# Optimization experiments

Hardware: AMD Instinct MI355X
Metric: run time of the kernel (lower is better)

The kernel has to match this reference:

```python
import jax, jax.numpy as jnp
import numpy as np

B, S, D = 16384, 50, 256
H2 = D // 2  # att_fc1 output = hidden_size // 2

def setup_inputs() -> dict:
    key = jax.random.key(0)
    k1, k2, k3, k4, k5, k6 = jax.random.split(key, 6)
    user_news_vecs = jax.random.normal(k1, (B, S, D), dtype=jnp.float32)
    log_mask = jax.random.randint(k2, (B, S), 0, 2, dtype=jnp.int32)
    # learned params
    pad_doc = jax.random.uniform(k3, (1, D), dtype=jnp.float32, minval=-1.0, maxval=1.0)
    lim1 = 1.0 / np.sqrt(D)
    W1 = jax.random.uniform(k4, (D, H2), dtype=jnp.float32, minval=-lim1, maxval=lim1)
    b1 = jnp.zeros((H2,), dtype=jnp.float32)
    lim2 = 1.0 / np.sqrt(H2)
    W2 = jax.random.uniform(k5, (H2, 1), dtype=jnp.float32, minval=-lim2, maxval=lim2)
    b2 = jnp.zeros((1,), dtype=jnp.float32)
    return {"user_news_vecs": user_news_vecs, "log_mask": log_mask,
            "pad_doc": pad_doc, "W1": W1, "b1": b1, "W2": W2, "b2": b2}

def reference(user_news_vecs, log_mask, pad_doc, W1, b1, W2, b2):
    # use_mask=False branch of get_user_log_vec: replace masked-out slots with pad_doc
    m = log_mask.astype(user_news_vecs.dtype)[..., None]          # [B,S,1]
    x = user_news_vecs * m + pad_doc[None, :, :] * (1.0 - m)      # [B,S,D]
    # AttentionPooling with attn_mask=None
    e = jnp.tanh(jnp.einsum('bsd,dh->bsh', x, W1) + b1)           # [B,S,H2]
    alpha = jnp.exp(jnp.einsum('bsh,ho->bso', e, W2) + b2)        # [B,S,1]
    alpha = alpha / (jnp.sum(alpha, axis=1, keepdims=True) + 1e-8)
    out = jnp.einsum('bsd,bso->bd', x, alpha)                     # [B,D]
    return out
```

## Files before the change

### kernel.cpp

```cpp
#include <hip/hip_runtime.h>

#define BB 16384
#define SS 50
#define DD 256
#define HH 128

typedef __attribute__((ext_vector_type(8))) __bf16 bf16x8;
typedef __attribute__((ext_vector_type(4))) float f32x4;

__global__ __launch_bounds__(256) void prep_w1(const float* __restrict__ W1,
                                               __bf16* __restrict__ w1t) {
    int idx = blockIdx.x * 256 + threadIdx.x;
    int n = idx >> 8;
    int k = idx & 255;
    w1t[n * 256 + k] = (__bf16)W1[k * HH + n];
}

template <bool USE_WS>
__global__ __launch_bounds__(256, 4) void user_enc(
    const float* __restrict__ vecs,
    const int*   __restrict__ lmask,
    const float* __restrict__ pad,
    const float* __restrict__ b1,
    const float* __restrict__ W2,
    const float* __restrict__ b2,
    const __bf16* __restrict__ w1t,
    const float* __restrict__ W1f,
    float* __restrict__ out)
{
    __shared__ float s_alpha[SS];
    __shared__ float s_m[SS];
    __shared__ __align__(16) float s_part[256 * 4];
    __shared__ float s_sum[4], s_pad[4];

    const int b    = blockIdx.x;
    const int t    = threadIdx.x;
    const int wid  = t >> 6;
    const int lane = t & 63;
    const int lo16 = lane & 15;
    const int q    = lane >> 4;
    const int r    = (wid << 4) + lo16;

    bool act = false;
    if (r < SS) act = (lmask[b * SS + r] != 0);
    if (q == 0 && r < SS) s_m[r] = act ? 1.0f : 0.0f;

    const float* vrowp = vecs + (size_t)b * (SS * DD) + (size_t)r * DD;
    bf16x8 afr[8];
    #pragma unroll
    for (int kk = 0; kk < 8; ++kk) {
        const float* src = pad + kk * 32 + q * 8;
        float4 lo = *(const float4*)(src);
        float4 hi = *(const float4*)(src + 4);
        bf16x8 f;
        f[0] = (__bf16)lo.x; f[1] = (__bf16)lo.y; f[2] = (__bf16)lo.z; f[3] = (__bf16)lo.w;
        f[4] = (__bf16)hi.x; f[5] = (__bf16)hi.y; f[6] = (__bf16)hi.z; f[7] = (__bf16)hi.w;
        afr[kk] = f;
    }
    if (act) {
        #pragma unroll
        for (int kk = 0; kk < 8; ++kk) {
            const float* src = vrowp + kk * 32 + q * 8;
            float4 lo = *(const float4*)(src);
            float4 hi = *(const float4*)(src + 4);
            bf16x8 f;
            f[0] = (__bf16)lo.x; f[1] = (__bf16)lo.y; f[2] = (__bf16)lo.z; f[3] = (__bf16)lo.w;
            f[4] = (__bf16)hi.x; f[5] = (__bf16)hi.y; f[6] = (__bf16)hi.z; f[7] = (__bf16)hi.w;
            afr[kk] = f;
        }
    }

    const float b2v = b2[0];
    float zacc[4] = {0.f, 0.f, 0.f, 0.f};

    #pragma unroll
    for (int nt = 0; nt < 8; ++nt) {
        const int c = (nt << 4) + lo16;
        f32x4 acc = {0.f, 0.f, 0.f, 0.f};
        #pragma unroll
        for (int kk = 0; kk < 8; ++kk) {
            bf16x8 bfr;
            if constexpr (USE_WS) {
                bfr = *(const bf16x8*)(w1t + c * 256 + kk * 32 + q * 8);
            } else {
                #pragma unroll
                for (int j = 0; j < 8; ++j)
                    bfr[j] = (__bf16)W1f[(kk * 32 + q * 8 + j) * HH + c];
            }
            acc = __builtin_amdgcn_mfma_f32_16x16x32_bf16(afr[kk], bfr, acc, 0, 0, 0);
        }
        const float b1c = b1[c];
        const float w2c = W2[c];
        #pragma unroll
        for (int i = 0; i < 4; ++i) {
            float y = acc[i] + b1c;
            y = fminf(fmaxf(y, -15.f), 15.f);
            float ex = __expf(2.f * y);
            float th = (ex - 1.f) * __builtin_amdgcn_rcpf(ex + 1.f);
            zacc[i] += th * w2c;
        }
    }

    #pragma unroll
    for (int i = 0; i < 4; ++i) {
        float z = zacc[i];
        z += __shfl_xor(z, 1);
        z += __shfl_xor(z, 2);
        z += __shfl_xor(z, 4);
        z += __shfl_xor(z, 8);
        if (lo16 == 0) {
            int srow = (wid << 4) + (q << 2) + i;
            if (srow < SS) s_alpha[srow] = __expf(z + b2v);
        }
    }
    __syncthreads();

    float4 acc4 = {0.f, 0.f, 0.f, 0.f};
    float asum = 0.f, apad = 0.f;
    const float* vb = vecs + (size_t)b * (SS * DD);
    for (int s = wid; s < SS; s += 4) {
        float a = s_alpha[s];
        asum += a;
        if (s_m[s] != 0.0f) {
            float4 xv = *(const float4*)(vb + s * DD + lane * 4);
            acc4.x += a * xv.x;
            acc4.y += a * xv.y;
            acc4.z += a * xv.z;
            acc4.w += a * xv.w;
        } else {
            apad += a;
        }
    }
    *(float4*)&s_part[t * 4] = acc4;
    if (lane == 0) { s_sum[wid] = asum; s_pad[wid] = apad; }
    __syncthreads();

    if (t < 64) {
        float4 p0 = *(const float4*)&s_part[(0 * 64 + t) * 4];
        float4 p1 = *(const float4*)&s_part[(1 * 64 + t) * 4];
        float4 p2 = *(const float4*)&s_part[(2 * 64 + t) * 4];
        float4 p3 = *(const float4*)&s_part[(3 * 64 + t) * 4];
        float denom = s_sum[0] + s_sum[1] + s_sum[2] + s_sum[3] + 1e-8f;
        float ptot  = s_pad[0] + s_pad[1] + s_pad[2] + s_pad[3];
        float inv = 1.0f / denom;
        float4 pd = *(const float4*)(pad + t * 4);
        float4 o;
        o.x = (p0.x + p1.x + p2.x + p3.x + ptot * pd.x) * inv;
        o.y = (p0.y + p1.y + p2.y + p3.y + ptot * pd.y) * inv;
        o.z = (p0.z + p1.z + p2.z + p3.z + ptot * pd.z) * inv;
        o.w = (p0.w + p1.w + p2.w + p3.w + ptot * pd.w) * inv;
        *(float4*)(out + (size_t)b * DD + t * 4) = o;
    }
}

extern "C" void kernel_launch(void* const* d_in, const int* in_sizes, int n_in,
                              void* d_out, int out_size, void* d_ws, size_t ws_size,
                              hipStream_t stream) {
    const float* vecs  = (const float*)d_in[0];
    const int*   lmask = (const int*)d_in[1];
    const float* pad   = (const float*)d_in[2];
    const float* W1    = (const float*)d_in[3];
    const float* b1    = (const float*)d_in[4];
    const float* W2    = (const float*)d_in[5];
    const float* b2    = (const float*)d_in[6];
    float* out = (float*)d_out;

    if (ws_size >= (size_t)(HH * DD * sizeof(__bf16))) {
        __bf16* w1t = (__bf16*)d_ws;
        prep_w1<<<dim3(HH * DD / 256), dim3(256), 0, stream>>>(W1, w1t);
        user_enc<true><<<dim3(BB), dim3(256), 0, stream>>>(vecs, lmask, pad, b1, W2, b2,
                                                           w1t, W1, out);
    } else {
        user_enc<false><<<dim3(BB), dim3(256), 0, stream>>>(vecs, lmask, pad, b1, W2, b2,
                                                            nullptr, W1, out);
    }
}
```

Baseline: 1.416 ms.

## Process batches in pairs per block with persistent loop, precomputed pad alpha, prefetch

Each block now walks 16 batch rows in pairs instead of handling one row, so every W1 fragment load feeds two MFMAs. The attention logit for pad rows is computed once by a small prep kernel and substituted directly, which skips loading pad vectors into the A fragments. The next pair's vecs rows are touched early to warm the cache. The costs are higher register pressure from the doubled accumulators and fragments, and a grid 16x smaller, which may reduce latency hiding.

```diff
diff --git a/kernel.cpp b/kernel.cpp
--- a/kernel.cpp
+++ b/kernel.cpp
@@ -4,6 +4,8 @@
 #define SS 50
 #define DD 256
 #define HH 128
+#define NB 16
+#define GRID (BB / NB)
 
 typedef __attribute__((ext_vector_type(8))) __bf16 bf16x8;
 typedef __attribute__((ext_vector_type(4))) float f32x4;
@@ -14,6 +16,24 @@
     int n = idx >> 8;
     int k = idx & 255;
     w1t[n * 256 + k] = (__bf16)W1[k * HH + n];
+}
+
+__global__ __launch_bounds__(128) void prep_pad(const float* __restrict__ pad,
+                                                const float* __restrict__ W1,
+                                                const float* __restrict__ b1,
+                                                const float* __restrict__ W2,
+                                                const float* __restrict__ b2,
+                                                float* __restrict__ apad) {
+    __shared__ float s2[2];
+    const int h = threadIdx.x;
+    float a = b1[h];
+    for (int k = 0; k < DD; ++k) a = fmaf(pad[k], W1[k * HH + h], a);
+    float v = tanhf(a) * W2[h];
+    #pragma unroll
+    for (int off = 1; off < 64; off <<= 1) v += __shfl_xor(v, off);
+    if ((h & 63) == 0) s2[h >> 6] = v;
+    __syncthreads();
+    if (h == 0) apad[0] = __expf(s2[0] + s2[1] + b2[0]);
 }
 
 template <bool USE_WS>
@@ -26,14 +46,14 @@
     const float* __restrict__ b2,
     const __bf16* __restrict__ w1t,
     const float* __restrict__ W1f,
+    const float* __restrict__ apad_ws,
     float* __restrict__ out)
 {
-    __shared__ float s_alpha[SS];
-    __shared__ float s_m[SS];
-    __shared__ __align__(16) float s_part[256 * 4];
-    __shared__ float s_sum[4], s_pad[4];
-
-    const int b    = blockIdx.x;
+    __shared__ float s_alpha[2][SS];
+    __shared__ float s_m[2][SS];
+    __shared__ __align__(16) float s_part[2][256 * 4];
+    __shared__ float s_sum[2][4], s_pad2[2][4];
+
     const int t    = threadIdx.x;
     const int wid  = t >> 6;
     const int lane = t & 63;
@@ -41,115 +61,196 @@
     const int q    = lane >> 4;
     const int r    = (wid << 4) + lo16;
 
-    bool act = false;
-    if (r < SS) act = (lmask[b * SS + r] != 0);
-    if (q == 0 && r < SS) s_m[r] = act ? 1.0f : 0.0f;
-
-    const float* vrowp = vecs + (size_t)b * (SS * DD) + (size_t)r * DD;
-    bf16x8 afr[8];
+    const float b2v   = b2[0];
+    const float apadv = USE_WS ? apad_ws[0] : 0.0f;
+    const int   bbase = blockIdx.x * NB;
+
+    bool act[2];
     #pragma unroll
-    for (int kk = 0; kk < 8; ++kk) {
-        const float* src = pad + kk * 32 + q * 8;
-        float4 lo = *(const float4*)(src);
-        float4 hi = *(const float4*)(src + 4);
-        bf16x8 f;
-        f[0] = (__bf16)lo.x; f[1] = (__bf16)lo.y; f[2] = (__bf16)lo.z; f[3] = (__bf16)lo.w;
-        f[4] = (__bf16)hi.x; f[5] = (__bf16)hi.y; f[6] = (__bf16)hi.z; f[7] = (__bf16)hi.w;
-        afr[kk] = f;
-    }
-    if (act) {
-        #pragma unroll
-        for (int kk = 0; kk < 8; ++kk) {
-            const float* src = vrowp + kk * 32 + q * 8;
-            float4 lo = *(const float4*)(src);
-            float4 hi = *(const float4*)(src + 4);
-            bf16x8 f;
-            f[0] = (__bf16)lo.x; f[1] = (__bf16)lo.y; f[2] = (__bf16)lo.z; f[3] = (__bf16)lo.w;
-            f[4] = (__bf16)hi.x; f[5] = (__bf16)hi.y; f[6] = (__bf16)hi.z; f[7] = (__bf16)hi.w;
-            afr[kk] = f;
-        }
-    }
-
-    const float b2v = b2[0];
-    float zacc[4] = {0.f, 0.f, 0.f, 0.f};
-
-    #pragma unroll
-    for (int nt = 0; nt < 8; ++nt) {
-        const int c = (nt << 4) + lo16;
-        f32x4 acc = {0.f, 0.f, 0.f, 0.f};
-        #pragma unroll
-        for (int kk = 0; kk < 8; ++kk) {
-            bf16x8 bfr;
+    for (int u = 0; u < 2; ++u)
+        act[u] = (r < SS) && (lmask[(size_t)(bbase + u) * SS + r] != 0);
+
+    for (int p = 0; p < NB / 2; ++p) {
+        const int b = bbase + 2 * p;
+        const float* vb0 = vecs + (size_t)b * (SS * DD);
+        const float* vb1 = vb0 + SS * DD;
+
+        bf16x8 afr[2][8];
+        #pragma unroll
+        for (int u = 0; u < 2; ++u) {
+            const float* vrowp = (u ? vb1 : vb0) + (size_t)r * DD;
             if constexpr (USE_WS) {
-                bfr = *(const bf16x8*)(w1t + c * 256 + kk * 32 + q * 8);
+                #pragma unroll
+                for (int kk = 0; kk < 8; ++kk) {
+                    bf16x8 f;
+                    #pragma unroll
+                    for (int j = 0; j < 8; ++j) f[j] = (__bf16)0.0f;
+                    afr[u][kk] = f;
+                }
+                if (act[u]) {
+                    #pragma unroll
+                    for (int kk = 0; kk < 8; ++kk) {
+                        const float* src = vrowp + kk * 32 + q * 8;
+                        float4 lo = *(const float4*)(src);
+                        float4 hi = *(const float4*)(src + 4);
+                        bf16x8 f;
+                        f[0] = (__bf16)lo.x; f[1] = (__bf16)lo.y; f[2] = (__bf16)lo.z; f[3] = (__bf16)lo.w;
+                        f[4] = (__bf16)hi.x; f[5] = (__bf16)hi.y; f[6] = (__bf16)hi.z; f[7] = (__bf16)hi.w;
+                        afr[u][kk] = f;
+                    }
+                }
             } else {
                 #pragma unroll
-                for (int j = 0; j < 8; ++j)
-                    bfr[j] = (__bf16)W1f[(kk * 32 + q * 8 + j) * HH + c];
-            }
-            acc = __builtin_amdgcn_mfma_f32_16x16x32_bf16(afr[kk], bfr, acc, 0, 0, 0);
-        }
-        const float b1c = b1[c];
-        const float w2c = W2[c];
+                for (int kk = 0; kk < 8; ++kk) {
+                    const float* src = pad + kk * 32 + q * 8;
+                    float4 lo = *(const float4*)(src);
+                    float4 hi = *(const float4*)(src + 4);
+                    bf16x8 f;
+                    f[0] = (__bf16)lo.x; f[1] = (__bf16)lo.y; f[2] = (__bf16)lo.z; f[3] = (__bf16)lo.w;
+                    f[4] = (__bf16)hi.x; f[5] = (__bf16)hi.y; f[6] = (__bf16)hi.z; f[7] = (__bf16)hi.w;
+                    afr[u][kk] = f;
+                }
+                if (act[u]) {
+                    #pragma unroll
+                    for (int kk = 0; kk < 8; ++kk) {
+                        const float* src = vrowp + kk * 32 + q * 8;
+                        float4 lo = *(const float4*)(src);
+                        float4 hi = *(const float4*)(src + 4);
+                        bf16x8 f;
+                        f[0] = (__bf16)lo.x; f[1] = (__bf16)lo.y; f[2] = (__bf16)lo.z; f[3] = (__bf16)lo.w;
+                        f[4] = (__bf16)hi.x; f[5] = (__bf16)hi.y; f[6] = (__bf16)hi.z; f[7] = (__bf16)hi.w;
+                        afr[u][kk] = f;
+                    }
+                }
+            }
+        }
+        if (q == 0 && r < SS) {
+            s_m[0][r] = act[0] ? 1.0f : 0.0f;
+            s_m[1][r] = act[1] ? 1.0f : 0.0f;
+        }
+
+        bool actn[2] = {false, false};
+        float tch[8] = {0.f, 0.f, 0.f, 0.f, 0.f, 0.f, 0.f, 0.f};
+        if (p + 1 < NB / 2) {
+            #pragma unroll
+            for (int u = 0; u < 2; ++u) {
+                actn[u] = (r < SS) && (lmask[(size_t)(b + 2 + u) * SS + r] != 0);
+                if (actn[u]) {
+                    const float* vn = vecs + (size_t)(b + 2 + u) * (SS * DD) + (size_t)r * DD;
+                    #pragma unroll
+                    for (int j = 0; j < 4; ++j)
+                        tch[u * 4 + j] = vn[(q * 4 + j) * 16];
+                }
+            }
+        }
+
+        float zacc[2][4] = {{0.f,0.f,0.f,0.f},{0.f,0.f,0.f,0.f}};
+        #pragma unroll
+        for (int nt = 0; nt < 8; ++nt) {
+            const int c = (nt << 4) + lo16;
+            f32x4 acc0 = {0.f,0.f,0.f,0.f};
+            f32x4 acc1 = {0.f,0.f,0.f,0.f};
+            #pragma unroll
+            for (int kk = 0; kk < 8; ++kk) {
+                bf16x8 bfr;
+                if constexpr (USE_WS) {
+                    bfr = *(const bf16x8*)(w1t + c * 256 + kk * 32 + q * 8);
+                } else {
+                    #pragma unroll
+                    for (int j = 0; j < 8; ++j)
+                        bfr[j] = (__bf16)W1f[(kk * 32 + q * 8 + j) * HH + c];
+                }
+                acc0 = __builtin_amdgcn_mfma_f32_16x16x32_bf16(afr[0][kk], bfr, acc0, 0, 0, 0);
+                acc1 = __builtin_amdgcn_mfma_f32_16x16x32_bf16(afr[1][kk], bfr, acc1, 0, 0, 0);
+            }
+            const float b1c = b1[c];
+            const float w2c = W2[c];
+            #pragma unroll
+            for (int i = 0; i < 4; ++i) {
+                {
+                    float y = acc0[i] + b1c;
+                    y = fminf(fmaxf(y, -15.f), 15.f);
+                    float ex = __expf(2.f * y);
+                    zacc[0][i] += (ex - 1.f) * __builtin_amdgcn_rcpf(ex + 1.f) * w2c;
+                }
+                {
+                    float y = acc1[i] + b1c;
+                    y = fminf(fmaxf(y, -15.f), 15.f);
+                    float ex = __expf(2.f * y);
+                    zacc[1][i] += (ex - 1.f) * __builtin_amdgcn_rcpf(ex + 1.f) * w2c;
+                }
+            }
+        }
+
+        const float actf0 = act[0] ? 1.f : 0.f;
+        const float actf1 = act[1] ? 1.f : 0.f;
         #pragma unroll
         for (int i = 0; i < 4; ++i) {
-            float y = acc[i] + b1c;
-            y = fminf(fmaxf(y, -15.f), 15.f);
-            float ex = __expf(2.f * y);
-            float th = (ex - 1.f) * __builtin_amdgcn_rcpf(ex + 1.f);
-            zacc[i] += th * w2c;
-        }
-    }
-
-    #pragma unroll
-    for (int i = 0; i < 4; ++i) {
-        float z = zacc[i];
-        z += __shfl_xor(z, 1);
-        z += __shfl_xor(z, 2);
-        z += __shfl_xor(z, 4);
-        z += __shfl_xor(z, 8);
-        if (lo16 == 0) {
-            int srow = (wid << 4) + (q << 2) + i;
-            if (srow < SS) s_alpha[srow] = __expf(z + b2v);
-        }
-    }
-    __syncthreads();
-
-    float4 acc4 = {0.f, 0.f, 0.f, 0.f};
-    float asum = 0.f, apad = 0.f;
-    const float* vb = vecs + (size_t)b * (SS * DD);
-    for (int s = wid; s < SS; s += 4) {
-        float a = s_alpha[s];
-        asum += a;
-        if (s_m[s] != 0.0f) {
-            float4 xv = *(const float4*)(vb + s * DD + lane * 4);
-            acc4.x += a * xv.x;
-            acc4.y += a * xv.y;
-            acc4.z += a * xv.z;
-            acc4.w += a * xv.w;
-        } else {
-            apad += a;
-        }
-    }
-    *(float4*)&s_part[t * 4] = acc4;
-    if (lane == 0) { s_sum[wid] = asum; s_pad[wid] = apad; }
-    __syncthreads();
-
-    if (t < 64) {
-        float4 p0 = *(const float4*)&s_part[(0 * 64 + t) * 4];
-        float4 p1 = *(const float4*)&s_part[(1 * 64 + t) * 4];
-        float4 p2 = *(const float4*)&s_part[(2 * 64 + t) * 4];
-        float4 p3 = *(const float4*)&s_part[(3 * 64 + t) * 4];
-        float denom = s_sum[0] + s_sum[1] + s_sum[2] + s_sum[3] + 1e-8f;
-        float ptot  = s_pad[0] + s_pad[1] + s_pad[2] + s_pad[3];
-        float inv = 1.0f / denom;
-        float4 pd = *(const float4*)(pad + t * 4);
-        float4 o;
-        o.x = (p0.x + p1.x + p2.x + p3.x + ptot * pd.x) * inv;
-        o.y = (p0.y + p1.y + p2.y + p3.y + ptot * pd.y) * inv;
-        o.z = (p0.z + p1.z + p2.z + p3.z + ptot * pd.z) * inv;
-        o.w = (p0.w + p1.w + p2.w + p3.w + ptot * pd.w) * inv;
-        *(float4*)(out + (size_t)b * DD + t * 4) = o;
+            float z0 = zacc[0][i], z1 = zacc[1][i];
+            z0 += __shfl_xor(z0, 1); z0 += __shfl_xor(z0, 2);
+            z0 += __shfl_xor(z0, 4); z0 += __shfl_xor(z0, 8);
+            z1 += __shfl_xor(z1, 1); z1 += __shfl_xor(z1, 2);
+            z1 += __shfl_xor(z1, 4); z1 += __shfl_xor(z1, 8);
+            const int srow = (wid << 4) + (q << 2) + i;
+            const float a0 = __shfl(actf0, (q << 2) + i);
+            const float a1 = __shfl(actf1, (q << 2) + i);
+            if (lo16 == 0 && srow < SS) {
+                if constexpr (USE_WS) {
+                    s_alpha[0][srow] = (a0 != 0.f) ? __expf(z0 + b2v) : apadv;
+                    s_alpha[1][srow] = (a1 != 0.f) ? __expf(z1 + b2v) : apadv;
+                } else {
+                    s_alpha[0][srow] = __expf(z0 + b2v);
+                    s_alpha[1][srow] = __expf(z1 + b2v);
+                }
+            }
+        }
+
+        asm volatile("" :: "v"(tch[0]), "v"(tch[1]), "v"(tch[2]), "v"(tch[3]),
+                           "v"(tch[4]), "v"(tch[5]), "v"(tch[6]), "v"(tch[7]));
+        __syncthreads();
+
+        #pragma unroll
+        for (int u = 0; u < 2; ++u) {
+            const float* vbu = u ? vb1 : vb0;
+            float4 acc4 = {0.f, 0.f, 0.f, 0.f};
+            float asum = 0.f, apacc = 0.f;
+            for (int s = wid; s < SS; s += 4) {
+                float a = s_alpha[u][s];
+                asum += a;
+                if (s_m[u][s] != 0.0f) {
+                    float4 xv = *(const float4*)(vbu + s * DD + lane * 4);
+                    acc4.x += a * xv.x;
+                    acc4.y += a * xv.y;
+                    acc4.z += a * xv.z;
+                    acc4.w += a * xv.w;
+                } else {
+                    apacc += a;
+                }
+            }
+            *(float4*)&s_part[u][t * 4] = acc4;
+            if (lane == 0) { s_sum[u][wid] = asum; s_pad2[u][wid] = apacc; }
+        }
+        __syncthreads();
+
+        if (wid < 2) {
+            const int u = wid;
+            float4 p0 = *(const float4*)&s_part[u][(0 * 64 + lane) * 4];
+            float4 p1 = *(const float4*)&s_part[u][(1 * 64 + lane) * 4];
+            float4 p2 = *(const float4*)&s_part[u][(2 * 64 + lane) * 4];
+            float4 p3 = *(const float4*)&s_part[u][(3 * 64 + lane) * 4];
+            float denom = s_sum[u][0] + s_sum[u][1] + s_sum[u][2] + s_sum[u][3] + 1e-8f;
+            float ptot  = s_pad2[u][0] + s_pad2[u][1] + s_pad2[u][2] + s_pad2[u][3];
+            float inv = 1.0f / denom;
+            float4 pd = *(const float4*)(pad + lane * 4);
+            float4 o;
+            o.x = (p0.x + p1.x + p2.x + p3.x + ptot * pd.x) * inv;
+            o.y = (p0.y + p1.y + p2.y + p3.y + ptot * pd.y) * inv;
+            o.z = (p0.z + p1.z + p2.z + p3.z + ptot * pd.z) * inv;
+            o.w = (p0.w + p1.w + p2.w + p3.w + ptot * pd.w) * inv;
+            *(float4*)(out + (size_t)(b + u) * DD + lane * 4) = o;
+        }
+        act[0] = actn[0];
+        act[1] = actn[1];
     }
 }
 
@@ -165,13 +266,16 @@
     const float* b2    = (const float*)d_in[6];
     float* out = (float*)d_out;
 
-    if (ws_size >= (size_t)(HH * DD * sizeof(__bf16))) {
+    const size_t w1t_bytes = (size_t)HH * DD * sizeof(__bf16);
+    if (ws_size >= w1t_bytes + 16) {
         __bf16* w1t = (__bf16*)d_ws;
+        float*  apad = (float*)((char*)d_ws + w1t_bytes);
         prep_w1<<<dim3(HH * DD / 256), dim3(256), 0, stream>>>(W1, w1t);
-        user_enc<true><<<dim3(BB), dim3(256), 0, stream>>>(vecs, lmask, pad, b1, W2, b2,
-                                                           w1t, W1, out);
+        prep_pad<<<dim3(1), dim3(128), 0, stream>>>(pad, W1, b1, W2, b2, apad);
+        user_enc<true><<<dim3(GRID), dim3(256), 0, stream>>>(vecs, lmask, pad, b1, W2, b2,
+                                                             w1t, W1, apad, out);
     } else {
-        user_enc<false><<<dim3(BB), dim3(256), 0, stream>>>(vecs, lmask, pad, b1, W2, b2,
-                                                            nullptr, W1, out);
+        user_enc<false><<<dim3(GRID), dim3(256), 0, stream>>>(vecs, lmask, pad, b1, W2, b2,
+                                                              nullptr, W1, nullptr, out);
     }
 }
```

Result: slower. 1.853 ms (+30.9%).

## Process 16 batches per block with register-resident W1 and LDS-staged X tiles

Applied to the files above, without the earlier changes.

Each block now loops over 16 batch rows. W1 fragments stay in registers for the whole block, and each batch row's X is staged as bf16 in swizzled LDS. Each wave computes 32 hidden columns across all 64 padded rows, which removes the repeated per-block W1 loads. Masked rows skip the global read and use a precomputed pad-row alpha produced by a new tiny kernel. The cost is a large LDS footprint (about 32KB bf16 tile), lower occupancy, and more synchronisation inside each batch iteration.

```diff
diff --git a/kernel.cpp b/kernel.cpp
--- a/kernel.cpp
+++ b/kernel.cpp
@@ -4,6 +4,8 @@
 #define SS 50
 #define DD 256
 #define HH 128
+#define NB 16
+#define GRID (BB / NB)
 
 typedef __attribute__((ext_vector_type(8))) __bf16 bf16x8;
 typedef __attribute__((ext_vector_type(4))) float f32x4;
@@ -16,8 +18,26 @@
     w1t[n * 256 + k] = (__bf16)W1[k * HH + n];
 }
 
+__global__ __launch_bounds__(128) void prep_pad(const float* __restrict__ pad,
+                                                const float* __restrict__ W1,
+                                                const float* __restrict__ b1,
+                                                const float* __restrict__ W2,
+                                                const float* __restrict__ b2,
+                                                float* __restrict__ apad) {
+    __shared__ float s2[2];
+    const int h = threadIdx.x;
+    float a = b1[h];
+    for (int k = 0; k < DD; ++k) a = fmaf(pad[k], W1[k * HH + h], a);
+    float v = tanhf(a) * W2[h];
+    #pragma unroll
+    for (int off = 1; off < 64; off <<= 1) v += __shfl_xor(v, off);
+    if ((h & 63) == 0) s2[h >> 6] = v;
+    __syncthreads();
+    if (h == 0) apad[0] = __expf(s2[0] + s2[1] + b2[0]);
+}
+
 template <bool USE_WS>
-__global__ __launch_bounds__(256, 4) void user_enc(
+__global__ __launch_bounds__(256) void user_enc(
     const float* __restrict__ vecs,
     const int*   __restrict__ lmask,
     const float* __restrict__ pad,
@@ -26,130 +46,167 @@
     const float* __restrict__ b2,
     const __bf16* __restrict__ w1t,
     const float* __restrict__ W1f,
+    const float* __restrict__ apad_ws,
     float* __restrict__ out)
 {
-    __shared__ float s_alpha[SS];
-    __shared__ float s_m[SS];
+    __shared__ __align__(16) __bf16 s_x[64 * 256];
+    __shared__ float s_z[4][64];
+    __shared__ float s_alpha[64];
+    __shared__ float s_m[64];
     __shared__ __align__(16) float s_part[256 * 4];
-    __shared__ float s_sum[4], s_pad[4];
-
-    const int b    = blockIdx.x;
+    __shared__ float s_sum[4], s_apad[4];
+
     const int t    = threadIdx.x;
     const int wid  = t >> 6;
     const int lane = t & 63;
     const int lo16 = lane & 15;
     const int q    = lane >> 4;
-    const int r    = (wid << 4) + lo16;
-
-    bool act = false;
-    if (r < SS) act = (lmask[b * SS + r] != 0);
-    if (q == 0 && r < SS) s_m[r] = act ? 1.0f : 0.0f;
-
-    const float* vrowp = vecs + (size_t)b * (SS * DD) + (size_t)r * DD;
-    bf16x8 afr[8];
-    #pragma unroll
-    for (int kk = 0; kk < 8; ++kk) {
-        const float* src = pad + kk * 32 + q * 8;
-        float4 lo = *(const float4*)(src);
-        float4 hi = *(const float4*)(src + 4);
-        bf16x8 f;
-        f[0] = (__bf16)lo.x; f[1] = (__bf16)lo.y; f[2] = (__bf16)lo.z; f[3] = (__bf16)lo.w;
-        f[4] = (__bf16)hi.x; f[5] = (__bf16)hi.y; f[6] = (__bf16)hi.z; f[7] = (__bf16)hi.w;
-        afr[kk] = f;
-    }
-    if (act) {
+
+    const float b2v   = b2[0];
+    const float apadv = USE_WS ? apad_ws[0] : 0.0f;
+
+    const int c0 = wid * 32 + lo16;
+    const int c1 = c0 + 16;
+    const float b1c0 = b1[c0], b1c1 = b1[c1];
+    const float w2c0 = W2[c0], w2c1 = W2[c1];
+
+    bf16x8 bfr0[8], bfr1[8];
+    if constexpr (USE_WS) {
         #pragma unroll
         for (int kk = 0; kk < 8; ++kk) {
-            const float* src = vrowp + kk * 32 + q * 8;
-            float4 lo = *(const float4*)(src);
-            float4 hi = *(const float4*)(src + 4);
-            bf16x8 f;
-            f[0] = (__bf16)lo.x; f[1] = (__bf16)lo.y; f[2] = (__bf16)lo.z; f[3] = (__bf16)lo.w;
-            f[4] = (__bf16)hi.x; f[5] = (__bf16)hi.y; f[6] = (__bf16)hi.z; f[7] = (__bf16)hi.w;
-            afr[kk] = f;
-        }
-    }
-
-    const float b2v = b2[0];
-    float zacc[4] = {0.f, 0.f, 0.f, 0.f};
-
-    #pragma unroll
-    for (int nt = 0; nt < 8; ++nt) {
-        const int c = (nt << 4) + lo16;
-        f32x4 acc = {0.f, 0.f, 0.f, 0.f};
+            bfr0[kk] = *(const bf16x8*)(w1t + (size_t)c0 * 256 + kk * 32 + q * 8);
+            bfr1[kk] = *(const bf16x8*)(w1t + (size_t)c1 * 256 + kk * 32 + q * 8);
+        }
+    } else {
         #pragma unroll
         for (int kk = 0; kk < 8; ++kk) {
-            bf16x8 bfr;
-            if constexpr (USE_WS) {
-                bfr = *(const bf16x8*)(w1t + c * 256 + kk * 32 + q * 8);
-            } else {
+            bf16x8 f0, f1;
+            #pragma unroll
+            for (int j = 0; j < 8; ++j) {
+                f0[j] = (__bf16)W1f[(kk * 32 + q * 8 + j) * HH + c0];
+                f1[j] = (__bf16)W1f[(kk * 32 + q * 8 + j) * HH + c1];
+            }
+            bfr0[kk] = f0; bfr1[kk] = f1;
+        }
+    }
+
+    for (int i = t; i < 14 * 32; i += 256) {
+        int r = 50 + (i >> 5);
+        int c16 = i & 31;
+        *(f32x4*)((char*)s_x + r * 512 + ((c16 ^ (r & 7)) << 4)) = f32x4{0.f, 0.f, 0.f, 0.f};
+    }
+
+    const int bbase = blockIdx.x * NB;
+    const int sr = t >> 2;
+    const int sc = (t & 3) * 64;
+
+    for (int p = 0; p < NB; ++p) {
+        const int b = bbase + p;
+        const float* vb = vecs + (size_t)b * (SS * DD);
+
+        if (t < SS) s_m[t] = (lmask[(size_t)b * SS + t] != 0) ? 1.0f : 0.0f;
+
+        if (sr < SS) {
+            const bool act = (lmask[(size_t)b * SS + sr] != 0);
+            const float* src = nullptr;
+            if (act)               src = vb + sr * DD + sc;
+            else if constexpr (!USE_WS) src = pad + sc;
+            if (src) {
+                const int c16b = sc >> 3;
+                const int swz  = sr & 7;
                 #pragma unroll
-                for (int j = 0; j < 8; ++j)
-                    bfr[j] = (__bf16)W1f[(kk * 32 + q * 8 + j) * HH + c];
-            }
-            acc = __builtin_amdgcn_mfma_f32_16x16x32_bf16(afr[kk], bfr, acc, 0, 0, 0);
-        }
-        const float b1c = b1[c];
-        const float w2c = W2[c];
+                for (int jj = 0; jj < 8; ++jj) {
+                    float4 lo = *(const float4*)(src + jj * 8);
+                    float4 hi = *(const float4*)(src + jj * 8 + 4);
+                    bf16x8 f;
+                    f[0] = (__bf16)lo.x; f[1] = (__bf16)lo.y; f[2] = (__bf16)lo.z; f[3] = (__bf16)lo.w;
+                    f[4] = (__bf16)hi.x; f[5] = (__bf16)hi.y; f[6] = (__bf16)hi.z; f[7] = (__bf16)hi.w;
+                    *(bf16x8*)((char*)s_x + sr * 512 + (((c16b + jj) ^ swz) << 4)) = f;
+                }
+            }
+        }
+        __syncthreads();
+
         #pragma unroll
-        for (int i = 0; i < 4; ++i) {
-            float y = acc[i] + b1c;
-            y = fminf(fmaxf(y, -15.f), 15.f);
-            float ex = __expf(2.f * y);
-            float th = (ex - 1.f) * __builtin_amdgcn_rcpf(ex + 1.f);
-            zacc[i] += th * w2c;
-        }
-    }
-
-    #pragma unroll
-    for (int i = 0; i < 4; ++i) {
-        float z = zacc[i];
-        z += __shfl_xor(z, 1);
-        z += __shfl_xor(z, 2);
-        z += __shfl_xor(z, 4);
-        z += __shfl_xor(z, 8);
-        if (lo16 == 0) {
-            int srow = (wid << 4) + (q << 2) + i;
-            if (srow < SS) s_alpha[srow] = __expf(z + b2v);
-        }
-    }
-    __syncthreads();
-
-    float4 acc4 = {0.f, 0.f, 0.f, 0.f};
-    float asum = 0.f, apad = 0.f;
-    const float* vb = vecs + (size_t)b * (SS * DD);
-    for (int s = wid; s < SS; s += 4) {
-        float a = s_alpha[s];
-        asum += a;
-        if (s_m[s] != 0.0f) {
-            float4 xv = *(const float4*)(vb + s * DD + lane * 4);
-            acc4.x += a * xv.x;
-            acc4.y += a * xv.y;
-            acc4.z += a * xv.z;
-            acc4.w += a * xv.w;
-        } else {
-            apad += a;
-        }
-    }
-    *(float4*)&s_part[t * 4] = acc4;
-    if (lane == 0) { s_sum[wid] = asum; s_pad[wid] = apad; }
-    __syncthreads();
-
-    if (t < 64) {
-        float4 p0 = *(const float4*)&s_part[(0 * 64 + t) * 4];
-        float4 p1 = *(const float4*)&s_part[(1 * 64 + t) * 4];
-        float4 p2 = *(const float4*)&s_part[(2 * 64 + t) * 4];
-        float4 p3 = *(const float4*)&s_part[(3 * 64 + t) * 4];
-        float denom = s_sum[0] + s_sum[1] + s_sum[2] + s_sum[3] + 1e-8f;
-        float ptot  = s_pad[0] + s_pad[1] + s_pad[2] + s_pad[3];
-        float inv = 1.0f / denom;
-        float4 pd = *(const float4*)(pad + t * 4);
-        float4 o;
-        o.x = (p0.x + p1.x + p2.x + p3.x + ptot * pd.x) * inv;
-        o.y = (p0.y + p1.y + p2.y + p3.y + ptot * pd.y) * inv;
-        o.z = (p0.z + p1.z + p2.z + p3.z + ptot * pd.z) * inv;
-        o.w = (p0.w + p1.w + p2.w + p3.w + ptot * pd.w) * inv;
-        *(float4*)(out + (size_t)b * DD + t * 4) = o;
+        for (int mt = 0; mt < 4; ++mt) {
+            f32x4 acc0 = {0.f, 0.f, 0.f, 0.f};
+            f32x4 acc1 = {0.f, 0.f, 0.f, 0.f};
+            const int row = mt * 16 + lo16;
+            const int swz = row & 7;
+            #pragma unroll
+            for (int kk = 0; kk < 8; ++kk) {
+                const int c16 = (kk * 4 + q) ^ swz;
+                bf16x8 a = *(const bf16x8*)((const char*)s_x + row * 512 + (c16 << 4));
+                acc0 = __builtin_amdgcn_mfma_f32_16x16x32_bf16(a, bfr0[kk], acc0, 0, 0, 0);
+                acc1 = __builtin_amdgcn_mfma_f32_16x16x32_bf16(a, bfr1[kk], acc1, 0, 0, 0);
+            }
+            #pragma unroll
+            for (int i = 0; i < 4; ++i) {
+                float y0 = acc0[i] + b1c0;
+                y0 = fminf(fmaxf(y0, -15.f), 15.f);
+                float e0 = __expf(2.f * y0);
+                float z  = (e0 - 1.f) * __builtin_amdgcn_rcpf(e0 + 1.f) * w2c0;
+                float y1 = acc1[i] + b1c1;
+                y1 = fminf(fmaxf(y1, -15.f), 15.f);
+                float e1 = __expf(2.f * y1);
+                z += (e1 - 1.f) * __builtin_amdgcn_rcpf(e1 + 1.f) * w2c1;
+                z += __shfl_xor(z, 1);
+                z += __shfl_xor(z, 2);
+                z += __shfl_xor(z, 4);
+                z += __shfl_xor(z, 8);
+                if (lo16 == 0) s_z[wid][mt * 16 + (q << 2) + i] = z;
+            }
+        }
+        __syncthreads();
+
+        if (t < SS) {
+            float z4 = s_z[0][t] + s_z[1][t] + s_z[2][t] + s_z[3][t];
+            float al;
+            if constexpr (USE_WS)
+                al = (s_m[t] != 0.f) ? __expf(z4 + b2v) : apadv;
+            else
+                al = __expf(z4 + b2v);
+            s_alpha[t] = al;
+        }
+        __syncthreads();
+
+        {
+            float4 acc4 = {0.f, 0.f, 0.f, 0.f};
+            float asum = 0.f, apacc = 0.f;
+            for (int s = wid; s < SS; s += 4) {
+                float a = s_alpha[s];
+                asum += a;
+                if (s_m[s] != 0.0f) {
+                    float4 xv = *(const float4*)(vb + s * DD + lane * 4);
+                    acc4.x += a * xv.x;
+                    acc4.y += a * xv.y;
+                    acc4.z += a * xv.z;
+                    acc4.w += a * xv.w;
+                } else {
+                    apacc += a;
+                }
+            }
+            *(float4*)&s_part[t * 4] = acc4;
+            if (lane == 0) { s_sum[wid] = asum; s_apad[wid] = apacc; }
+        }
+        __syncthreads();
+
+        if (t < 64) {
+            float4 p0 = *(const float4*)&s_part[(0 * 64 + t) * 4];
+            float4 p1 = *(const float4*)&s_part[(1 * 64 + t) * 4];
+            float4 p2 = *(const float4*)&s_part[(2 * 64 + t) * 4];
+            float4 p3 = *(const float4*)&s_part[(3 * 64 + t) * 4];
+            float denom = s_sum[0] + s_sum[1] + s_sum[2] + s_sum[3] + 1e-8f;
+            float ptot  = s_apad[0] + s_apad[1] + s_apad[2] + s_apad[3];
+            float inv = 1.0f / denom;
+            float4 pd = *(const float4*)(pad + t * 4);
+            float4 o;
+            o.x = (p0.x + p1.x + p2.x + p3.x + ptot * pd.x) * inv;
+            o.y = (p0.y + p1.y + p2.y + p3.y + ptot * pd.y) * inv;
+            o.z = (p0.z + p1.z + p2.z + p3.z + ptot * pd.z) * inv;
+            o.w = (p0.w + p1.w + p2.w + p3.w + ptot * pd.w) * inv;
+            *(float4*)(out + (size_t)b * DD + t * 4) = o;
+        }
     }
 }
 
@@ -165,13 +222,16 @@
     const float* b2    = (const float*)d_in[6];
     float* out = (float*)d_out;
 
-    if (ws_size >= (size_t)(HH * DD * sizeof(__bf16))) {
+    const size_t w1t_bytes = (size_t)HH * DD * sizeof(__bf16);
+    if (ws_size >= w1t_bytes + 16) {
         __bf16* w1t = (__bf16*)d_ws;
+        float*  apad = (float*)((char*)d_ws + w1t_bytes);
         prep_w1<<<dim3(HH * DD / 256), dim3(256), 0, stream>>>(W1, w1t);
-        user_enc<true><<<dim3(BB), dim3(256), 0, stream>>>(vecs, lmask, pad, b1, W2, b2,
-                                                           w1t, W1, out);
+        prep_pad<<<dim3(1), dim3(128), 0, stream>>>(pad, W1, b1, W2, b2, apad);
+        user_enc<true><<<dim3(GRID), dim3(256), 0, stream>>>(vecs, lmask, pad, b1, W2, b2,
+                                                             w1t, W1, apad, out);
     } else {
-        user_enc<false><<<dim3(BB), dim3(256), 0, stream>>>(vecs, lmask, pad, b1, W2, b2,
-                                                            nullptr, W1, out);
-    }
-}
+        user_enc<false><<<dim3(GRID), dim3(256), 0, stream>>>(vecs, lmask, pad, b1, W2, b2,
+                                                              nullptr, W1, nullptr, out);
+    }
+}
```

Measured after the change: 1.218 ms. 1.16x faster.
